# Kernel optimization log

Measured on AMD Instinct MI355X. Metric: run time of the kernel, lower is better.

## Reference

```python
import jax, jax.numpy as jnp
import numpy as np

B, C, HI, WI = 16, 256, 64, 64
DT = 512
NH = 8
EPS = 1e-5

def setup_inputs():
    key = jax.random.key(0)
    ks = jax.random.split(key, 16)
    def w(k, shape):
        return jax.random.normal(k, shape, jnp.float32) * 0.02
    return {
        'F_vis': jax.random.normal(ks[0], (B, C, HI, WI), jnp.float32),
        'F_text': jax.random.normal(ks[1], (B, DT), jnp.float32),
        'F_unified': jax.random.normal(ks[2], (B, DT), jnp.float32),
        'F_teacher': jax.random.normal(ks[3], (B, DT), jnp.float32),
        'tp_w1': w(ks[4], (DT, C)), 'tp_b1': jnp.zeros((C,), jnp.float32),
        'tp_w2': w(ks[5], (C, C)), 'tp_b2': jnp.zeros((C,), jnp.float32),
        'q_w': w(ks[6], (C, C)), 'q_b': jnp.zeros((C,), jnp.float32),
        'k_w': w(ks[7], (C, C)), 'k_b': jnp.zeros((C,), jnp.float32),
        'v_w': w(ks[8], (C, C)), 'v_b': jnp.zeros((C,), jnp.float32),
        'o_w': w(ks[9], (C, C)), 'o_b': jnp.zeros((C,), jnp.float32),
        'fa_w': w(ks[10], (DT, 1)), 'fa_b': jnp.zeros((1,), jnp.float32),
        'gp_w': w(ks[11], (DT, C)), 'gp_b': jnp.zeros((C,), jnp.float32),
        'ln_g': jnp.ones((C,), jnp.float32), 'ln_b': jnp.zeros((C,), jnp.float32),
    }

def reference(F_vis, F_text, F_unified, F_teacher, tp_w1, tp_b1, tp_w2, tp_b2, q_w, q_b, k_w, k_b, v_w, v_b, o_w, o_b, fa_w, fa_b, gp_w, gp_b, ln_g, ln_b):
    b, c, h, w_ = F_vis.shape
    T = h * w_
    hd = c // NH
    x = F_vis.reshape(b, c, T).transpose(0, 2, 1)  # [B,T,C] vision tokens
    # text projection -> single query (T_q = 1)
    t = jax.nn.gelu(F_text @ tp_w1 + tp_b1, approximate=False) @ tp_w2 + tp_b2  # [B,C]
    q = (t @ q_w + q_b).reshape(b, NH, hd)                       # [B,H,hd]
    kh = (x @ k_w + k_b).reshape(b, T, NH, hd)                   # [B,T,H,hd]
    vh = (x @ v_w + v_b).reshape(b, T, NH, hd)
    scores = jnp.einsum('bhd,bthd->bht', q, kh) * (hd ** -0.5)   # [B,H,T]
    attn = jax.nn.softmax(scores, axis=-1)                        # dropout = identity at eval
    z = jnp.einsum('bht,bthd->bhd', attn, vh).reshape(b, c)      # [B,C]
    z = z @ o_w + o_b                                             # out_proj once; expand is a broadcast of identical rows
    # student-teacher joint gate
    f_stack = jnp.stack([F_unified, F_teacher], axis=1)           # [B,2,DT]
    a = jax.nn.softmax(f_stack @ fa_w + fa_b, axis=1)             # [B,2,1]
    f_cond = jnp.sum(a * f_stack, axis=1)                         # [B,DT]
    g = jax.nn.sigmoid(f_cond @ gp_w + gp_b)                      # [B,C]
    # residual + gated fusion + LayerNorm over channel dim
    y = x + g[:, None, :] * z[:, None, :]                         # [B,T,C]
    mu = jnp.mean(y, axis=-1, keepdims=True)
    var = jnp.var(y, axis=-1, keepdims=True)
    y = (y - mu) * jax.lax.rsqrt(var + EPS) * ln_g + ln_b
    out = y.transpose(0, 2, 1).reshape(b, c, h, w_)
    return out, attn[:, :, None, :]  # attn_weights [B,H,1,T] as in torch
```

## Files before the change

kernel.cpp:

```cpp
#include <hip/hip_runtime.h>
#include <math.h>

#define B_  16
#define C_  256
#define T_  4096
#define DT_ 512
#define NH_ 8
#define HD_ 32

__global__ __launch_bounds__(512) void k_t1gate(
    const float* __restrict__ F_text, const float* __restrict__ U,
    const float* __restrict__ Tt,
    const float* __restrict__ tp_w1, const float* __restrict__ tp_b1,
    const float* __restrict__ fa_w,  const float* __restrict__ fa_b,
    const float* __restrict__ gp_w,  const float* __restrict__ gp_b,
    float* __restrict__ t1, float* __restrict__ gout)
{
    __shared__ float xs[8192];
    __shared__ float part[8192];
    __shared__ float pd[2][16][32];
    __shared__ float a0s[16], a1s[16];
    int tid = threadIdx.x;
    int c0  = blockIdx.x * 16;
    int cl  = tid & 15, ks = tid >> 4;
    int c   = c0 + cl;

    for (int idx = tid; idx < 8192; idx += 512) xs[idx] = F_text[idx];
    __syncthreads();
    {
        float acc[16];
        #pragma unroll
        for (int b = 0; b < 16; ++b) acc[b] = 0.f;
        const float* wp = tp_w1 + (size_t)(ks * 16) * 256 + c;
        #pragma unroll
        for (int i = 0; i < 16; ++i) {
            float w = wp[(size_t)i * 256];
            int xi = ks * 16 + i;
            #pragma unroll
            for (int b = 0; b < 16; ++b) acc[b] += xs[b * 512 + xi] * w;
        }
        #pragma unroll
        for (int b = 0; b < 16; ++b) part[ks * 256 + b * 16 + cl] = acc[b];
    }
    __syncthreads();
    if (tid < 256) {
        int b = tid >> 4, cc = tid & 15;
        float s = 0.f;
        #pragma unroll
        for (int k2 = 0; k2 < 32; ++k2) s += part[k2 * 256 + b * 16 + cc];
        s += tp_b1[c0 + cc];
        s = 0.5f * s * (1.0f + erff(s * 0.70710678118654752f));
        t1[b * 256 + c0 + cc] = s;
    }
    __syncthreads();

    {
        int b = tid >> 5, sl = tid & 31;
        const float* ub = U  + b * 512 + sl * 16;
        const float* tb = Tt + b * 512 + sl * 16;
        const float* fw = fa_w + sl * 16;
        float su = 0.f, st = 0.f;
        #pragma unroll
        for (int j = 0; j < 16; ++j) { su += ub[j] * fw[j]; st += tb[j] * fw[j]; }
        pd[0][b][sl] = su; pd[1][b][sl] = st;
    }
    __syncthreads();
    if (tid < 16) {
        float s0 = fa_b[0], s1 = fa_b[0];
        #pragma unroll
        for (int sl = 0; sl < 32; ++sl) { s0 += pd[0][tid][sl]; s1 += pd[1][tid][sl]; }
        float mm = fmaxf(s0, s1);
        float e0 = expf(s0 - mm), e1 = expf(s1 - mm);
        float inv = 1.0f / (e0 + e1);
        a0s[tid] = e0 * inv; a1s[tid] = e1 * inv;
    }
    __syncthreads();
    for (int idx = tid; idx < 8192; idx += 512) {
        int b = idx >> 9;
        xs[idx] = a0s[b] * U[idx] + a1s[b] * Tt[idx];
    }
    __syncthreads();
    {
        float acc[16];
        #pragma unroll
        for (int b = 0; b < 16; ++b) acc[b] = 0.f;
        const float* wp = gp_w + (size_t)(ks * 16) * 256 + c;
        #pragma unroll
        for (int i = 0; i < 16; ++i) {
            float w = wp[(size_t)i * 256];
            int xi = ks * 16 + i;
            #pragma unroll
            for (int b = 0; b < 16; ++b) acc[b] += xs[b * 512 + xi] * w;
        }
        #pragma unroll
        for (int b = 0; b < 16; ++b) part[ks * 256 + b * 16 + cl] = acc[b];
    }
    __syncthreads();
    if (tid < 256) {
        int b = tid >> 4, cc = tid & 15;
        float s = 0.f;
        #pragma unroll
        for (int k2 = 0; k2 < 32; ++k2) s += part[k2 * 256 + b * 16 + cc];
        s += gp_b[c0 + cc];
        gout[b * 256 + c0 + cc] = 1.0f / (1.0f + expf(-s));
    }
}

template<int K, int ACT>
__global__ __launch_bounds__(512) void gemm16(const float* __restrict__ x,
                                              const float* __restrict__ W,
                                              const float* __restrict__ bias,
                                              float* __restrict__ out)
{
    __shared__ float xs[16 * K];
    __shared__ float part[32 * 256];
    int tid = threadIdx.x;
    int c0  = blockIdx.x * 16;

    for (int idx = tid; idx < 16 * K; idx += 512) xs[idx] = x[idx];
    __syncthreads();

    int cl = tid & 15, ks = tid >> 4;
    const int Kc = K / 32;
    int c = c0 + cl;

    float acc[16];
    #pragma unroll
    for (int b = 0; b < 16; ++b) acc[b] = 0.f;

    const float* wp = W + (size_t)(ks * Kc) * 256 + c;
    #pragma unroll
    for (int i = 0; i < Kc; ++i) {
        float w  = wp[(size_t)i * 256];
        int   xi = ks * Kc + i;
        #pragma unroll
        for (int b = 0; b < 16; ++b) acc[b] += xs[b * K + xi] * w;
    }
    #pragma unroll
    for (int b = 0; b < 16; ++b) part[ks * 256 + b * 16 + cl] = acc[b];
    __syncthreads();

    if (tid < 256) {
        int b = tid >> 4, cc = tid & 15;
        float s = 0.f;
        #pragma unroll
        for (int k2 = 0; k2 < 32; ++k2) s += part[k2 * 256 + b * 16 + cc];
        s += bias[c0 + cc];
        if (ACT == 1) s = 0.5f * s * (1.0f + erff(s * 0.70710678118654752f));
        out[b * 256 + c0 + cc] = s;
    }
}

__global__ __launch_bounds__(512) void k_qkq(const float* __restrict__ tv,
                                             const float* __restrict__ q_w,
                                             const float* __restrict__ q_b,
                                             const float* __restrict__ k_w,
                                             const float* __restrict__ k_b,
                                             float* __restrict__ kq,
                                             float* __restrict__ qkb)
{
    __shared__ float xs[4096];
    __shared__ float part[8192];
    __shared__ float qs[512];
    int tid = threadIdx.x;
    int h   = blockIdx.x;

    for (int idx = tid; idx < 4096; idx += 512) xs[idx] = tv[idx];
    __syncthreads();

    {
        int cl = tid & 31, ks = tid >> 5;
        float acc[16];
        #pragma unroll
        for (int b = 0; b < 16; ++b) acc[b] = 0.f;
        const float* wp = q_w + (size_t)(ks * 16) * 256 + h * HD_ + cl;
        #pragma unroll
        for (int i = 0; i < 16; ++i) {
            float w = wp[(size_t)i * 256];
            int xi = ks * 16 + i;
            #pragma unroll
            for (int b = 0; b < 16; ++b) acc[b] += xs[b * 256 + xi] * w;
        }
        #pragma unroll
        for (int b = 0; b < 16; ++b) part[(ks * 16 + b) * 32 + cl] = acc[b];
    }
    __syncthreads();
    {
        int b = tid >> 5, cl = tid & 31;
        float s = 0.f;
        #pragma unroll
        for (int k2 = 0; k2 < 16; ++k2) s += part[(k2 * 16 + b) * 32 + cl];
        qs[b * 32 + cl] = s + q_b[h * HD_ + cl];
    }
    __syncthreads();
    if (tid < 16) {
        float s = 0.f;
        #pragma unroll
        for (int d = 0; d < 32; ++d) s += qs[tid * 32 + d] * k_b[h * HD_ + d];
        qkb[tid * NH_ + h] = s;
    }

    {
        int c = tid >> 1, bh = tid & 1;
        const float4* kwp = reinterpret_cast<const float4*>(k_w + (size_t)c * 256 + h * HD_);
        float4 kw[8];
        #pragma unroll
        for (int j = 0; j < 8; ++j) kw[j] = kwp[j];
        float acc[8] = {0,0,0,0,0,0,0,0};
        #pragma unroll
        for (int j = 0; j < 8; ++j) {
            float w0 = kw[j].x, w1 = kw[j].y, w2 = kw[j].z, w3 = kw[j].w;
            #pragma unroll
            for (int bi = 0; bi < 8; ++bi) {
                const float* qp = &qs[(bh * 8 + bi) * 32 + j * 4];
                acc[bi] += qp[0] * w0 + qp[1] * w1 + qp[2] * w2 + qp[3] * w3;
            }
        }
        #pragma unroll
        for (int bi = 0; bi < 8; ++bi)
            kq[((size_t)((bh * 8 + bi) * NH_ + h)) * C_ + c] = acc[bi];
    }
}

__global__ __launch_bounds__(512) void k2_scores(const float* __restrict__ F_vis,
                                                 const float* __restrict__ kq,
                                                 const float* __restrict__ qkb,
                                                 float* __restrict__ e,
                                                 float* __restrict__ ms,
                                                 float* __restrict__ xac)
{
    int tc = blockIdx.x;
    int b  = blockIdx.y;
    int tid = threadIdx.x;
    int t0 = tc * 256;
    const float scale = 0.176776695296636893f;

    __shared__ float kqs[256][9];
    __shared__ __align__(16) float4 part4[8 * 8 * 64];
    __shared__ __align__(16) float esf[8 * 256];
    __shared__ float qkbs[8];
    __shared__ float redm[8][4], reds[8][4];

    for (int idx = tid; idx < 2048; idx += 512) {
        int c = idx & 255, h = idx >> 8;
        kqs[c][h] = kq[((size_t)(b * NH_ + h)) * C_ + c];
    }
    if (tid < 8) qkbs[tid] = qkb[b * NH_ + tid];
    __syncthreads();

    {
        int cs = tid >> 6, t4 = tid & 63;
        const float* fv = F_vis + ((size_t)b * C_) * T_ + t0 + t4 * 4;
        float4 acc[8];
        #pragma unroll
        for (int h = 0; h < 8; ++h) acc[h] = make_float4(0.f, 0.f, 0.f, 0.f);
        #pragma unroll 8
        for (int i = 0; i < 32; ++i) {
            int c = i * 8 + cs;
            float4 v = *reinterpret_cast<const float4*>(&fv[(size_t)c * T_]);
            #pragma unroll
            for (int h = 0; h < 8; ++h) {
                float w = kqs[c][h];
                acc[h].x += v.x * w; acc[h].y += v.y * w;
                acc[h].z += v.z * w; acc[h].w += v.w * w;
            }
        }
        #pragma unroll
        for (int h = 0; h < 8; ++h) part4[(cs * 8 + h) * 64 + t4] = acc[h];
    }
    __syncthreads();

    {
        int tl = tid & 255, hg = tid >> 8;
        int lane = tid & 63, wid = tid >> 6;
        const float* pf = reinterpret_cast<const float*>(part4);
        float sv[4], mh[4];
        #pragma unroll
        for (int hh = 0; hh < 4; ++hh) {
            int h = hg * 4 + hh;
            float s = 0.f;
            #pragma unroll
            for (int cs = 0; cs < 8; ++cs) s += pf[(cs * 8 + h) * 256 + tl];
            sv[hh] = (s + qkbs[h]) * scale;
            float m = sv[hh];
            #pragma unroll
            for (int o = 32; o; o >>= 1) m = fmaxf(m, __shfl_xor(m, o));
            mh[hh] = m;
        }
        if (lane == 0) {
            #pragma unroll
            for (int hh = 0; hh < 4; ++hh) redm[hg * 4 + hh][wid & 3] = mh[hh];
        }
        __syncthreads();
        float ev[4];
        #pragma unroll
        for (int hh = 0; hh < 4; ++hh) {
            int h = hg * 4 + hh;
            float m = fmaxf(fmaxf(redm[h][0], redm[h][1]), fmaxf(redm[h][2], redm[h][3]));
            ev[hh] = expf(sv[hh] - m);
            e[((size_t)(b * NH_ + h)) * T_ + t0 + tl] = ev[hh];
            esf[h * 256 + tl] = ev[hh];
            float sm = ev[hh];
            #pragma unroll
            for (int o = 32; o; o >>= 1) sm += __shfl_xor(sm, o);
            if (lane == 0) reds[h][wid & 3] = sm;
        }
        __syncthreads();
        if (tid < 8) {
            float m = fmaxf(fmaxf(redm[tid][0], redm[tid][1]),
                            fmaxf(redm[tid][2], redm[tid][3]));
            float sum = reds[tid][0] + reds[tid][1] + reds[tid][2] + reds[tid][3];
            size_t base = (((size_t)(b * NH_ + tid)) * 16 + tc) * 2;
            ms[base]     = m;
            ms[base + 1] = sum;
        }
    }

    {
        int lane = tid & 63, wid = tid >> 6;
        int cl = lane & 15, tq = lane >> 4;
        const float4* es4 = reinterpret_cast<const float4*>(esf);
        #pragma unroll
        for (int pass = 0; pass < 2; ++pass) {
            int c = pass * 128 + wid * 16 + cl;
            const float* fvc = F_vis + ((size_t)b * C_ + c) * T_ + t0;
            float p[8] = {0, 0, 0, 0, 0, 0, 0, 0};
            #pragma unroll 4
            for (int i = 0; i < 16; ++i) {
                int Q = tq * 16 + i;
                float4 v = *reinterpret_cast<const float4*>(&fvc[Q * 4]);
                #pragma unroll
                for (int h = 0; h < 8; ++h) {
                    float4 E = es4[h * 64 + Q];
                    p[h] += v.x * E.x + v.y * E.y + v.z * E.z + v.w * E.w;
                }
            }
            #pragma unroll
            for (int h = 0; h < 8; ++h) {
                p[h] += __shfl_xor(p[h], 16);
                p[h] += __shfl_xor(p[h], 32);
            }
            if (tq == 0) {
                #pragma unroll
                for (int h = 0; h < 8; ++h)
                    xac[(((size_t)tc * B_ + b) * NH_ + h) * C_ + c] = p[h];
            }
        }
    }
}

__global__ __launch_bounds__(256) void k5a_attn(const float* __restrict__ e,
                                                const float* __restrict__ ms,
                                                float* __restrict__ attn)
{
    int tc = blockIdx.x, b = blockIdx.y, tid = threadIdx.x;
    __shared__ float facts[8];
    if (tid < 8) {
        const float* mp = ms + ((size_t)(b * NH_ + tid)) * 32;
        float M = -1e30f;
        #pragma unroll
        for (int ck = 0; ck < 16; ++ck) M = fmaxf(M, mp[ck * 2]);
        float Z = 0.f;
        #pragma unroll
        for (int ck = 0; ck < 16; ++ck) Z += mp[ck * 2 + 1] * expf(mp[ck * 2] - M);
        facts[tid] = expf(mp[tc * 2] - M) / Z;
    }
    __syncthreads();
    #pragma unroll
    for (int idx = tid; idx < 512; idx += 256) {
        int h = idx >> 6, tq = idx & 63;
        const float4* ep = reinterpret_cast<const float4*>(
            e + ((size_t)(b * NH_ + h)) * T_ + tc * 256);
        float4* ap = reinterpret_cast<float4*>(
            attn + ((size_t)(b * NH_ + h)) * T_ + tc * 256);
        float f = facts[h];
        float4 a = ep[tq];
        a.x *= f; a.y *= f; a.z *= f; a.w *= f;
        ap[tq] = a;
    }
}

__global__ __launch_bounds__(1024) void k5b_gz(const float* __restrict__ ms,
                                               const float* __restrict__ xac,
                                               const float* __restrict__ v_w,
                                               const float* __restrict__ v_b,
                                               const float* __restrict__ o_w,
                                               const float* __restrict__ o_b,
                                               const float* __restrict__ g,
                                               float* __restrict__ gz)
{
    int b = blockIdx.x, tid = threadIdx.x;
    __shared__ float fact[8][16];
    __shared__ float xaL[2048];
    __shared__ float part[4][256];
    __shared__ float zp[256];
    __shared__ float Ms[8], iZs[8];

    if (tid < 8) {
        const float* mp = ms + ((size_t)(b * NH_ + tid)) * 32;
        float M = -1e30f;
        #pragma unroll
        for (int ck = 0; ck < 16; ++ck) M = fmaxf(M, mp[ck * 2]);
        float Z = 0.f;
        #pragma unroll
        for (int ck = 0; ck < 16; ++ck) Z += mp[ck * 2 + 1] * expf(mp[ck * 2] - M);
        Ms[tid] = M; iZs[tid] = 1.0f / Z;
    }
    __syncthreads();
    if (tid < 128) {
        int h = tid >> 4, ck = tid & 15;
        fact[h][ck] = expf(ms[((size_t)(b * NH_ + h)) * 32 + ck * 2] - Ms[h]) * iZs[h];
    }
    __syncthreads();

    for (int idx = tid; idx < 2048; idx += 1024) {
        int h = idx >> 8, c = idx & 255;
        float s = 0.f;
        #pragma unroll
        for (int ck = 0; ck < 16; ++ck)
            s += xac[(((size_t)ck * B_ + b) * NH_ + h) * C_ + c] * fact[h][ck];
        xaL[idx] = s;
    }
    __syncthreads();

    {
        int j = tid & 255, ks = tid >> 8;
        int h = j >> 5;
        float s = 0.f;
        #pragma unroll 8
        for (int c = ks * 64; c < ks * 64 + 64; ++c) s += xaL[h * 256 + c] * v_w[c * 256 + j];
        part[ks][j] = s;
    }
    __syncthreads();
    if (tid < 256)
        zp[tid] = part[0][tid] + part[1][tid] + part[2][tid] + part[3][tid] + v_b[tid];
    __syncthreads();
    {
        int j = tid & 255, ks = tid >> 8;
        float s = 0.f;
        #pragma unroll 8
        for (int i = ks * 64; i < ks * 64 + 64; ++i) s += zp[i] * o_w[i * 256 + j];
        part[ks][j] = s;
    }
    __syncthreads();
    if (tid < 256) {
        float z = part[0][tid] + part[1][tid] + part[2][tid] + part[3][tid] + o_b[tid];
        gz[b * 256 + tid] = g[b * 256 + tid] * z;
    }
}

__global__ __launch_bounds__(256) void k6_ln(const float* __restrict__ F_vis,
                                             const float* __restrict__ gz,
                                             const float* __restrict__ ln_g,
                                             const float* __restrict__ ln_b,
                                             float* __restrict__ out)
{
    int b  = blockIdx.y;
    int t0 = blockIdx.x * 32;
    int tid = threadIdx.x;
    int t4 = tid & 7;
    int cb = tid >> 3;

    __shared__ float gzs[256], lgs[256], lbs[256];
    __shared__ float4 redS[4][8], redQ[4][8];
    __shared__ float4 mu4s[8], rs4s[8];

    gzs[tid] = gz[b * C_ + tid];
    lgs[tid] = ln_g[tid];
    lbs[tid] = ln_b[tid];
    __syncthreads();

    const float* fvb = F_vis + (size_t)b * C_ * T_ + t0 + t4 * 4;
    float4 v[8];
    float4 s = make_float4(0.f, 0.f, 0.f, 0.f);
    float4 q = make_float4(0.f, 0.f, 0.f, 0.f);
    #pragma unroll
    for (int k = 0; k < 8; ++k) {
        int c = cb + k * 32;
        float4 x = *reinterpret_cast<const float4*>(&fvb[(size_t)c * T_]);
        float gc = gzs[c];
        x.x += gc; x.y += gc; x.z += gc; x.w += gc;
        v[k] = x;
        s.x += x.x; s.y += x.y; s.z += x.z; s.w += x.w;
        q.x += x.x * x.x; q.y += x.y * x.y; q.z += x.z * x.z; q.w += x.w * x.w;
    }
    #pragma unroll
    for (int o = 8; o <= 32; o <<= 1) {
        s.x += __shfl_xor(s.x, o); s.y += __shfl_xor(s.y, o);
        s.z += __shfl_xor(s.z, o); s.w += __shfl_xor(s.w, o);
        q.x += __shfl_xor(q.x, o); q.y += __shfl_xor(q.y, o);
        q.z += __shfl_xor(q.z, o); q.w += __shfl_xor(q.w, o);
    }
    int wid = tid >> 6;
    if ((tid & 63) < 8) { redS[wid][t4] = s; redQ[wid][t4] = q; }
    __syncthreads();
    if (tid < 8) {
        float4 S = redS[0][tid], Q = redQ[0][tid];
        #pragma unroll
        for (int w = 1; w < 4; ++w) {
            float4 a = redS[w][tid], c2 = redQ[w][tid];
            S.x += a.x; S.y += a.y; S.z += a.z; S.w += a.w;
            Q.x += c2.x; Q.y += c2.y; Q.z += c2.z; Q.w += c2.w;
        }
        float4 mu, rs;
        mu.x = S.x * (1.0f / C_); mu.y = S.y * (1.0f / C_);
        mu.z = S.z * (1.0f / C_); mu.w = S.w * (1.0f / C_);
        rs.x = rsqrtf(fmaxf(Q.x * (1.0f / C_) - mu.x * mu.x, 0.f) + 1e-5f);
        rs.y = rsqrtf(fmaxf(Q.y * (1.0f / C_) - mu.y * mu.y, 0.f) + 1e-5f);
        rs.z = rsqrtf(fmaxf(Q.z * (1.0f / C_) - mu.z * mu.z, 0.f) + 1e-5f);
        rs.w = rsqrtf(fmaxf(Q.w * (1.0f / C_) - mu.w * mu.w, 0.f) + 1e-5f);
        mu4s[tid] = mu; rs4s[tid] = rs;
    }
    __syncthreads();
    float4 mu = mu4s[t4], rs = rs4s[t4];
    float* ob = out + (size_t)b * C_ * T_ + t0 + t4 * 4;
    #pragma unroll
    for (int k = 0; k < 8; ++k) {
        int c = cb + k * 32;
        float lg = lgs[c], lb = lbs[c];
        float4 o;
        o.x = (v[k].x - mu.x) * rs.x * lg + lb;
        o.y = (v[k].y - mu.y) * rs.y * lg + lb;
        o.z = (v[k].z - mu.z) * rs.z * lg + lb;
        o.w = (v[k].w - mu.w) * rs.w * lg + lb;
        *reinterpret_cast<float4*>(&ob[(size_t)c * T_]) = o;
    }
}

extern "C" void kernel_launch(void* const* d_in, const int* in_sizes, int n_in,
                              void* d_out, int out_size, void* d_ws, size_t ws_size,
                              hipStream_t stream)
{
    const float* F_vis     = (const float*)d_in[0];
    const float* F_text    = (const float*)d_in[1];
    const float* F_unified = (const float*)d_in[2];
    const float* F_teacher = (const float*)d_in[3];
    const float* tp_w1 = (const float*)d_in[4];
    const float* tp_b1 = (const float*)d_in[5];
    const float* tp_w2 = (const float*)d_in[6];
    const float* tp_b2 = (const float*)d_in[7];
    const float* q_w   = (const float*)d_in[8];
    const float* q_b   = (const float*)d_in[9];
    const float* k_w   = (const float*)d_in[10];
    const float* k_b   = (const float*)d_in[11];
    const float* v_w   = (const float*)d_in[12];
    const float* v_b   = (const float*)d_in[13];
    const float* o_w   = (const float*)d_in[14];
    const float* o_b   = (const float*)d_in[15];
    const float* fa_w  = (const float*)d_in[16];
    const float* fa_b  = (const float*)d_in[17];
    const float* gp_w  = (const float*)d_in[18];
    const float* gp_b  = (const float*)d_in[19];
    const float* ln_g  = (const float*)d_in[20];
    const float* ln_b  = (const float*)d_in[21];

    float* ws  = (float*)d_ws;
    float* t1  = ws;
    float* tv  = ws + 4096;
    float* kq  = ws + 8192;
    float* qkb = ws + 40960;
    float* g   = ws + 41088;
    float* gz  = ws + 45184;
    float* e   = ws + 49280;
    float* ms  = ws + 573568;
    float* xac = ws + 577664;

    float* out  = (float*)d_out;
    float* attn = out + (size_t)B_ * C_ * T_;

    k_t1gate<<<16, 512, 0, stream>>>(F_text, F_unified, F_teacher,
                                     tp_w1, tp_b1, fa_w, fa_b, gp_w, gp_b,
                                     t1, g);
    gemm16<256, 0><<<16, 512, 0, stream>>>(t1, tp_w2, tp_b2, tv);
    k_qkq<<<NH_, 512, 0, stream>>>(tv, q_w, q_b, k_w, k_b, kq, qkb);

    k2_scores<<<dim3(16, B_), 512, 0, stream>>>(F_vis, kq, qkb, e, ms, xac);
    k5a_attn<<<dim3(16, B_), 256, 0, stream>>>(e, ms, attn);
    k5b_gz<<<B_, 1024, 0, stream>>>(ms, xac, v_w, v_b, o_w, o_b, g, gz);
    k6_ln<<<dim3(128, B_), 256, 0, stream>>>(F_vis, gz, ln_g, ln_b, out);
}
```

Before: 88.68 us.

## Stream F_vis tiles into LDS with async double-buffered global_load_lds in scores kernel

Replaces the per-thread register-accumulated score projection with a double-buffered pipeline that uses global_load_lds to copy 32-channel F_vis slabs straight into shared memory while the previous slab is consumed. Each thread now owns one token and four heads, which removes the cross-warp partial-sum buffer and its reduction pass. The goal is to overlap global memory latency with compute and cut LDS traffic for partials. In exchange it adds a barrier per stage, relies on hand-written vmcnt waits, and does scalar LDS reads with broadcast kqs accesses, where the padding on kqs is removed.

```diff
diff --git a/kernel.cpp b/kernel.cpp
--- a/kernel.cpp
+++ b/kernel.cpp
@@ -235,8 +235,8 @@
     int t0 = tc * 256;
     const float scale = 0.176776695296636893f;
 
-    __shared__ float kqs[256][9];
-    __shared__ __align__(16) float4 part4[8 * 8 * 64];
+    __shared__ float kqs[256][8];
+    __shared__ __align__(16) float buf[2][32 * 256];
     __shared__ __align__(16) float esf[8 * 256];
     __shared__ float qkbs[8];
     __shared__ float redm[8][4], reds[8][4];
@@ -246,42 +246,57 @@
         kqs[c][h] = kq[((size_t)(b * NH_ + h)) * C_ + c];
     }
     if (tid < 8) qkbs[tid] = qkb[b * NH_ + tid];
-    __syncthreads();
-
-    {
-        int cs = tid >> 6, t4 = tid & 63;
-        const float* fv = F_vis + ((size_t)b * C_) * T_ + t0 + t4 * 4;
-        float4 acc[8];
-        #pragma unroll
-        for (int h = 0; h < 8; ++h) acc[h] = make_float4(0.f, 0.f, 0.f, 0.f);
+
+    int wid = tid >> 6, lane = tid & 63;
+    const float* fvb = F_vis + ((size_t)b * C_) * T_ + t0;
+
+    #pragma unroll
+    for (int j = 0; j < 4; ++j) {
+        const float* src = fvb + (size_t)(wid * 4 + j) * T_ + lane * 4;
+        __builtin_amdgcn_global_load_lds(
+            (const __attribute__((address_space(1))) void*)src,
+            (__attribute__((address_space(3))) void*)&buf[0][(wid * 4 + j) * 256],
+            16, 0, 0);
+    }
+    __syncthreads();
+
+    float sv[4] = {0.f, 0.f, 0.f, 0.f};
+    int t = tid & 255, hg = tid >> 8;
+    #pragma unroll
+    for (int s = 0; s < 8; ++s) {
+        if (s < 7) {
+            #pragma unroll
+            for (int j = 0; j < 4; ++j) {
+                int c = (s + 1) * 32 + wid * 4 + j;
+                const float* src = fvb + (size_t)c * T_ + lane * 4;
+                __builtin_amdgcn_global_load_lds(
+                    (const __attribute__((address_space(1))) void*)src,
+                    (__attribute__((address_space(3))) void*)&buf[(s + 1) & 1][(wid * 4 + j) * 256],
+                    16, 0, 0);
+            }
+            asm volatile("s_waitcnt vmcnt(4)" ::: "memory");
+        } else {
+            asm volatile("s_waitcnt vmcnt(0)" ::: "memory");
+        }
+        __builtin_amdgcn_sched_barrier(0);
+        __builtin_amdgcn_s_barrier();
+
+        const float* bb = &buf[s & 1][0];
         #pragma unroll 8
-        for (int i = 0; i < 32; ++i) {
-            int c = i * 8 + cs;
-            float4 v = *reinterpret_cast<const float4*>(&fv[(size_t)c * T_]);
-            #pragma unroll
-            for (int h = 0; h < 8; ++h) {
-                float w = kqs[c][h];
-                acc[h].x += v.x * w; acc[h].y += v.y * w;
-                acc[h].z += v.z * w; acc[h].w += v.w * w;
-            }
-        }
-        #pragma unroll
-        for (int h = 0; h < 8; ++h) part4[(cs * 8 + h) * 64 + t4] = acc[h];
-    }
-    __syncthreads();
-
-    {
-        int tl = tid & 255, hg = tid >> 8;
-        int lane = tid & 63, wid = tid >> 6;
-        const float* pf = reinterpret_cast<const float*>(part4);
-        float sv[4], mh[4];
+        for (int c = 0; c < 32; ++c) {
+            float v = bb[c * 256 + t];
+            #pragma unroll
+            for (int hh = 0; hh < 4; ++hh)
+                sv[hh] += v * kqs[s * 32 + c][hg * 4 + hh];
+        }
+        __builtin_amdgcn_s_barrier();
+    }
+
+    {
+        float mh[4];
         #pragma unroll
         for (int hh = 0; hh < 4; ++hh) {
-            int h = hg * 4 + hh;
-            float s = 0.f;
-            #pragma unroll
-            for (int cs = 0; cs < 8; ++cs) s += pf[(cs * 8 + h) * 256 + tl];
-            sv[hh] = (s + qkbs[h]) * scale;
+            sv[hh] = (sv[hh] + qkbs[hg * 4 + hh]) * scale;
             float m = sv[hh];
             #pragma unroll
             for (int o = 32; o; o >>= 1) m = fmaxf(m, __shfl_xor(m, o));
@@ -292,15 +307,14 @@
             for (int hh = 0; hh < 4; ++hh) redm[hg * 4 + hh][wid & 3] = mh[hh];
         }
         __syncthreads();
-        float ev[4];
         #pragma unroll
         for (int hh = 0; hh < 4; ++hh) {
             int h = hg * 4 + hh;
             float m = fmaxf(fmaxf(redm[h][0], redm[h][1]), fmaxf(redm[h][2], redm[h][3]));
-            ev[hh] = expf(sv[hh] - m);
-            e[((size_t)(b * NH_ + h)) * T_ + t0 + tl] = ev[hh];
-            esf[h * 256 + tl] = ev[hh];
-            float sm = ev[hh];
+            float ev = expf(sv[hh] - m);
+            e[((size_t)(b * NH_ + h)) * T_ + t0 + t] = ev;
+            esf[h * 256 + t] = ev;
+            float sm = ev;
             #pragma unroll
             for (int o = 32; o; o >>= 1) sm += __shfl_xor(sm, o);
             if (lane == 0) reds[h][wid & 3] = sm;
@@ -317,7 +331,6 @@
     }
 
     {
-        int lane = tid & 63, wid = tid >> 6;
         int cl = lane & 15, tq = lane >> 4;
         const float4* es4 = reinterpret_cast<const float4*>(esf);
         #pragma unroll
```

Result: slower. 92.01 us (+3.8%).
